# Performance work log

Hardware: AMD Instinct MI355X
Metric: run time of the kernel (lower is better)

The kernel has to match this reference:

```python
import jax, jax.numpy as jnp
import numpy as np

FIELD_SIZE = 26
EMBED_DIM = 32
# upper-triangular pair indices (i < j), order matches the torch double loop
_I, _J = np.triu_indices(FIELD_SIZE, k=1)
NUM_PAIRS = _I.shape[0]  # 325


def setup_inputs() -> dict:
    key = jax.random.key(0)
    k1, k2, k3 = jax.random.split(key, 3)
    B = 4096
    x = jax.random.normal(k1, (B, FIELD_SIZE, EMBED_DIM), dtype=jnp.float32)
    # torch Linear weight layout: [out_features, in_features]; y = v @ W.T + b
    W = jax.random.normal(k2, (NUM_PAIRS, EMBED_DIM, EMBED_DIM), dtype=jnp.float32) * (1.0 / np.sqrt(EMBED_DIM))
    b = jax.random.normal(k3, (NUM_PAIRS, EMBED_DIM), dtype=jnp.float32) * 0.01
    return {"x": x, "W": W, "b": b}


def reference(x, W, b):
    # x: [B, F, D]; W: [P, D, D] (torch layout, out x in); b: [P, D]
    i_idx = jnp.asarray(_I)
    j_idx = jnp.asarray(_J)
    v_i = x[:, i_idx, :]  # [B, P, D]
    v_j = x[:, j_idx, :]  # [B, P, D]
    # per-pair Linear: v_i @ W[p].T + b[p], fused with elementwise mul by v_j
    t = jnp.einsum('bpd,ped->bpe', v_i, W) + b[None, :, :]
    return t * v_j  # [B, P, D]
```

## Files before the change

### kernel.cpp

```cpp
#include <hip/hip_runtime.h>

constexpr int FIELD = 26;
constexpr int EDIM  = 32;
constexpr int NPAIR = 325;
constexpr int BT    = 16;

typedef __bf16 bf16x8 __attribute__((ext_vector_type(8)));
typedef float  f32x4  __attribute__((ext_vector_type(4)));

static __device__ inline bf16x8 cvt8(const float4 a, const float4 b) {
    bf16x8 r;
    r[0] = (__bf16)a.x; r[1] = (__bf16)a.y; r[2] = (__bf16)a.z; r[3] = (__bf16)a.w;
    r[4] = (__bf16)b.x; r[5] = (__bf16)b.y; r[6] = (__bf16)b.z; r[7] = (__bf16)b.w;
    return r;
}

__global__ __launch_bounds__(256, 4) void bilinear_persist(
    const float* __restrict__ x,
    const float* __restrict__ W,
    const float* __restrict__ bias,
    float* __restrict__ out,
    int ntiles)
{
    __shared__ float4 stage[4][BT][8];

    const int tid = threadIdx.x;
    const int w   = tid >> 6;
    const int l   = tid & 63;
    const int lr  = l & 15;
    const int g   = l >> 4;
    const int bq  = l >> 3;
    const int eq  = l & 7;

    const int stride = gridDim.x * 4;

    for (int idx = blockIdx.x * 4 + w; idx < ntiles; idx += stride) {
        const int bt = (int)(((unsigned long long)(unsigned)idx * 13215284ull) >> 32);
        const int p  = idx - bt * NPAIR;
        const int b0 = bt * BT;

        int fi = 0, rem = p;
        #pragma unroll 1
        while (rem >= FIELD - 1 - fi) { rem -= FIELD - 1 - fi; ++fi; }
        const int fj = fi + 1 + rem;

        const float* xp = x + ((size_t)(b0 + lr) * FIELD + fi) * EDIM + g * 8;
        const float4 xa = *(const float4*)xp;
        const float4 xb = *(const float4*)(xp + 4);
        float4 wlo[2], whi[2];
        #pragma unroll
        for (int n = 0; n < 2; ++n) {
            const float* wp = W + ((size_t)p * EDIM + n * 16 + lr) * EDIM + g * 8;
            wlo[n] = *(const float4*)wp;
            whi[n] = *(const float4*)(wp + 4);
        }
        const float4 b4 = *(const float4*)(bias + (size_t)p * EDIM + eq * 4);
        float4 xj4[2];
        #pragma unroll
        for (int s = 0; s < 2; ++s)
            xj4[s] = *(const float4*)(x + ((size_t)(b0 + bq + 8 * s) * FIELD + fj) * EDIM + eq * 4);

        const bf16x8 xf = cvt8(xa, xb);
        #pragma unroll
        for (int n = 0; n < 2; ++n) {
            const f32x4 acc = __builtin_amdgcn_mfma_f32_16x16x32_bf16(
                cvt8(wlo[n], whi[n]), xf, (f32x4){0.f, 0.f, 0.f, 0.f}, 0, 0, 0);
            float4 v; v.x = acc[0]; v.y = acc[1]; v.z = acc[2]; v.w = acc[3];
            stage[w][lr][(n * 4 + g) ^ (lr & 7)] = v;
        }

        #pragma unroll
        for (int s = 0; s < 2; ++s) {
            const int row = bq + 8 * s;
            const float4 t = stage[w][row][eq ^ (row & 7)];
            f32x4 r;
            r[0] = (t.x + b4.x) * xj4[s].x;
            r[1] = (t.y + b4.y) * xj4[s].y;
            r[2] = (t.z + b4.z) * xj4[s].z;
            r[3] = (t.w + b4.w) * xj4[s].w;
            f32x4* dst = (f32x4*)(out + ((size_t)(b0 + row) * NPAIR + p) * EDIM + eq * 4);
            __builtin_nontemporal_store(r, dst);
        }
    }
}

extern "C" void kernel_launch(void* const* d_in, const int* in_sizes, int n_in,
                              void* d_out, int out_size, void* d_ws, size_t ws_size,
                              hipStream_t stream) {
    const float* x    = (const float*)d_in[0];
    const float* W    = (const float*)d_in[1];
    const float* bias = (const float*)d_in[2];
    float* out        = (float*)d_out;

    const int B      = in_sizes[0] / (FIELD * EDIM);
    const int ntiles = (B / BT) * NPAIR;
    bilinear_persist<<<dim3(1024), dim3(256), 0, stream>>>(x, W, bias, out, ntiles);
}
```

Before: 75.15 us.

## Software-pipeline tile loads with double-buffered registers and LDS staging

Restructures the persistent loop so each wave loads the next tile's x, W, bias and x_j fragments into registers while it computes and stores the current tile, ping-ponging between two register fragment sets and two LDS staging buffers. The aim is to hide global load latency behind the MFMA and store work. The output stores also change from nontemporal builtins to plain float4 stores, which can change cache behaviour on this write-heavy kernel. Holding two fragment sets raises register pressure under the 256x4 launch bound.

```diff
diff --git a/kernel.cpp b/kernel.cpp
--- a/kernel.cpp
+++ b/kernel.cpp
@@ -15,14 +15,21 @@
     return r;
 }
 
-__global__ __launch_bounds__(256, 4) void bilinear_persist(
+struct Frag {
+    float4 xi0, xi1;
+    float4 w0, w1, w2, w3;
+    float4 b4;
+    float4 xj0, xj1;
+};
+
+__global__ __launch_bounds__(256, 4) void bilinear_pipe(
     const float* __restrict__ x,
     const float* __restrict__ W,
     const float* __restrict__ bias,
     float* __restrict__ out,
     int ntiles)
 {
-    __shared__ float4 stage[4][BT][8];
+    __shared__ float4 stage[4][2][BT][8];
 
     const int tid = threadIdx.x;
     const int w   = tid >> 6;
@@ -32,55 +39,68 @@
     const int bq  = l >> 3;
     const int eq  = l & 7;
 
-    const int stride = gridDim.x * 4;
-
-    for (int idx = blockIdx.x * 4 + w; idx < ntiles; idx += stride) {
+    auto load_tile = [&](int idx, Frag& f, int& p, int& b0) {
         const int bt = (int)(((unsigned long long)(unsigned)idx * 13215284ull) >> 32);
-        const int p  = idx - bt * NPAIR;
-        const int b0 = bt * BT;
-
+        p  = idx - bt * NPAIR;
+        b0 = bt * BT;
+        const float* wp0 = W + ((size_t)p * EDIM + lr) * EDIM + g * 8;
+        f.w0 = *(const float4*)wp0;
+        f.w1 = *(const float4*)(wp0 + 4);
+        const float* wp1 = wp0 + 16 * EDIM;
+        f.w2 = *(const float4*)wp1;
+        f.w3 = *(const float4*)(wp1 + 4);
+        f.b4 = *(const float4*)(bias + (size_t)p * EDIM + eq * 4);
         int fi = 0, rem = p;
         #pragma unroll 1
         while (rem >= FIELD - 1 - fi) { rem -= FIELD - 1 - fi; ++fi; }
         const int fj = fi + 1 + rem;
+        const float* xp = x + ((size_t)(b0 + lr) * FIELD + fi) * EDIM + g * 8;
+        f.xi0 = *(const float4*)xp;
+        f.xi1 = *(const float4*)(xp + 4);
+        f.xj0 = *(const float4*)(x + ((size_t)(b0 + bq)     * FIELD + fj) * EDIM + eq * 4);
+        f.xj1 = *(const float4*)(x + ((size_t)(b0 + bq + 8) * FIELD + fj) * EDIM + eq * 4);
+    };
 
-        const float* xp = x + ((size_t)(b0 + lr) * FIELD + fi) * EDIM + g * 8;
-        const float4 xa = *(const float4*)xp;
-        const float4 xb = *(const float4*)(xp + 4);
-        float4 wlo[2], whi[2];
-        #pragma unroll
-        for (int n = 0; n < 2; ++n) {
-            const float* wp = W + ((size_t)p * EDIM + n * 16 + lr) * EDIM + g * 8;
-            wlo[n] = *(const float4*)wp;
-            whi[n] = *(const float4*)(wp + 4);
-        }
-        const float4 b4 = *(const float4*)(bias + (size_t)p * EDIM + eq * 4);
-        float4 xj4[2];
-        #pragma unroll
-        for (int s = 0; s < 2; ++s)
-            xj4[s] = *(const float4*)(x + ((size_t)(b0 + bq + 8 * s) * FIELD + fj) * EDIM + eq * 4);
+    auto compute_store = [&](const Frag& f, int p, int b0, float4 (*stg)[8]) {
+        const bf16x8 xf = cvt8(f.xi0, f.xi1);
+        const f32x4 zero = {0.f, 0.f, 0.f, 0.f};
+        const f32x4 a0 = __builtin_amdgcn_mfma_f32_16x16x32_bf16(cvt8(f.w0, f.w1), xf, zero, 0, 0, 0);
+        float4 v0; v0.x = a0[0]; v0.y = a0[1]; v0.z = a0[2]; v0.w = a0[3];
+        stg[lr][g ^ (lr & 7)] = v0;
+        const f32x4 a1 = __builtin_amdgcn_mfma_f32_16x16x32_bf16(cvt8(f.w2, f.w3), xf, zero, 0, 0, 0);
+        float4 v1; v1.x = a1[0]; v1.y = a1[1]; v1.z = a1[2]; v1.w = a1[3];
+        stg[lr][(4 + g) ^ (lr & 7)] = v1;
+        const float4 t0 = stg[bq][eq ^ (bq & 7)];
+        const float4 t1 = stg[bq + 8][eq ^ (bq & 7)];
+        float4 r0, r1;
+        r0.x = (t0.x + f.b4.x) * f.xj0.x;  r0.y = (t0.y + f.b4.y) * f.xj0.y;
+        r0.z = (t0.z + f.b4.z) * f.xj0.z;  r0.w = (t0.w + f.b4.w) * f.xj0.w;
+        r1.x = (t1.x + f.b4.x) * f.xj1.x;  r1.y = (t1.y + f.b4.y) * f.xj1.y;
+        r1.z = (t1.z + f.b4.z) * f.xj1.z;  r1.w = (t1.w + f.b4.w) * f.xj1.w;
+        *(float4*)(out + ((size_t)(b0 + bq)     * NPAIR + p) * EDIM + eq * 4) = r0;
+        *(float4*)(out + ((size_t)(b0 + bq + 8) * NPAIR + p) * EDIM + eq * 4) = r1;
+    };
 
-        const bf16x8 xf = cvt8(xa, xb);
-        #pragma unroll
-        for (int n = 0; n < 2; ++n) {
-            const f32x4 acc = __builtin_amdgcn_mfma_f32_16x16x32_bf16(
-                cvt8(wlo[n], whi[n]), xf, (f32x4){0.f, 0.f, 0.f, 0.f}, 0, 0, 0);
-            float4 v; v.x = acc[0]; v.y = acc[1]; v.z = acc[2]; v.w = acc[3];
-            stage[w][lr][(n * 4 + g) ^ (lr & 7)] = v;
-        }
+    int idx = blockIdx.x * 4 + w;
+    const int stride = gridDim.x * 4;
+    if (idx >= ntiles) return;
 
-        #pragma unroll
-        for (int s = 0; s < 2; ++s) {
-            const int row = bq + 8 * s;
-            const float4 t = stage[w][row][eq ^ (row & 7)];
-            f32x4 r;
-            r[0] = (t.x + b4.x) * xj4[s].x;
-            r[1] = (t.y + b4.y) * xj4[s].y;
-            r[2] = (t.z + b4.z) * xj4[s].z;
-            r[3] = (t.w + b4.w) * xj4[s].w;
-            f32x4* dst = (f32x4*)(out + ((size_t)(b0 + row) * NPAIR + p) * EDIM + eq * 4);
-            __builtin_nontemporal_store(r, dst);
-        }
+    Frag A, B;
+    int pA, b0A, pB, b0B;
+    float4 (*stgA)[8] = stage[w][0];
+    float4 (*stgB)[8] = stage[w][1];
+
+    load_tile(idx, A, pA, b0A);
+    for (;;) {
+        const int i1 = idx + stride;
+        if (i1 < ntiles) load_tile(i1, B, pB, b0B);
+        compute_store(A, pA, b0A, stgA);
+        if (i1 >= ntiles) break;
+        const int i2 = i1 + stride;
+        if (i2 < ntiles) load_tile(i2, A, pA, b0A);
+        compute_store(B, pB, b0B, stgB);
+        if (i2 >= ntiles) break;
+        idx = i2;
     }
 }
 
@@ -94,5 +114,5 @@
 
     const int B      = in_sizes[0] / (FIELD * EDIM);
     const int ntiles = (B / BT) * NPAIR;
-    bilinear_persist<<<dim3(1024), dim3(256), 0, stream>>>(x, W, bias, out, ntiles);
+    bilinear_pipe<<<dim3(1024), dim3(256), 0, stream>>>(x, W, bias, out, ntiles);
 }
```

New measurement: 74.31 us. About the same (-1.1%).
